# Optimization experiments

Hardware: AMD Instinct MI355X
Metric: run time of the kernel (lower is better)

## Reference

```python
import jax, jax.numpy as jnp
import numpy as np
import math

B, L, OBS, ACT = 2, 1024, 64, 16
OE, AE, RE, TE = 512, 256, 128, 128
C, H, NL, FF = 1024, 16, 4, 4096
DH = C // H


def setup_inputs():
    key = jax.random.key(0)
    ks = jax.random.split(key, 20)
    def nrm(k, shape, std=1.0):
        return jax.random.normal(k, shape, jnp.float32) * std
    kb = jax.random.split(ks[19], 12)
    return {
        'obs_seq': nrm(ks[0], (B, L, OBS)),
        'act_seq': nrm(ks[1], (B, L, ACT)),
        'rew_seq': nrm(ks[2], (B, L, 1)),
        'obs_W': nrm(ks[3], (OBS, OE), OBS ** -0.5), 'obs_b': jnp.zeros((OE,)),
        'act_W': nrm(ks[4], (ACT, AE), ACT ** -0.5), 'act_b': jnp.zeros((AE,)),
        'rew_W': nrm(ks[5], (1, RE), 1.0), 'rew_b': jnp.zeros((RE,)),
        'tr_W': nrm(ks[6], (OBS, TE), OBS ** -0.5), 'tr_b': jnp.zeros((TE,)),
        'bn_gamma': jnp.ones((OBS,)), 'bn_beta': jnp.zeros((OBS,)),
        'ln1_w': jnp.ones((NL, C)), 'ln1_b': jnp.zeros((NL, C)),
        'qkv_W': nrm(kb[0], (NL, C, 3 * C), C ** -0.5), 'qkv_b': jnp.zeros((NL, 3 * C)),
        'out_W': nrm(kb[1], (NL, C, C), C ** -0.5), 'out_b': jnp.zeros((NL, C)),
        'ln2_w': jnp.ones((NL, C)), 'ln2_b': jnp.zeros((NL, C)),
        'fc_W': nrm(kb[2], (NL, C, FF), C ** -0.5), 'fc_b': jnp.zeros((NL, FF)),
        'pj_W': nrm(kb[3], (NL, FF, C), FF ** -0.5), 'pj_b': jnp.zeros((NL, C)),
    }


def _ln(x, w, b):
    m = x.mean(-1, keepdims=True)
    v = ((x - m) ** 2).mean(-1, keepdims=True)
    return (x - m) * jax.lax.rsqrt(v + 1e-5) * w + b


def _forward(obs_seq, act_seq, rew_seq, obs_W, obs_b, act_W, act_b, rew_W, rew_b,
             tr_W, tr_b, bn_gamma, bn_beta, ln1_w, ln1_b, qkv_W, qkv_b, out_W, out_b,
             ln2_w, ln2_b, fc_W, fc_b, pj_W, pj_b):
    # transition branch: prepend first obs, take deltas; BatchNorm1d in training
    # mode uses biased batch stats over (batch, time) per channel.
    full_obs = jnp.concatenate([obs_seq[:, :1], obs_seq], axis=1)  # (B, L+1, OBS)
    obs2 = full_obs[:, :-1]
    tran = full_obs[:, 1:] - full_obs[:, :-1]  # (B, L, OBS)
    tm = tran.mean((0, 1))
    tv = ((tran - tm) ** 2).mean((0, 1))
    tran = (tran - tm) * jax.lax.rsqrt(tv + 1e-5) * bn_gamma + bn_beta
    # encoder_activation is identity
    enc = jnp.concatenate([
        obs2 @ obs_W + obs_b,
        act_seq @ act_W + act_b,
        rew_seq @ rew_W + rew_b,
        tran @ tr_W + tr_b,
    ], axis=-1)  # (B, L, C)
    mask = jnp.tril(jnp.ones((L, L), dtype=bool))

    def block(x, p):
        l1w, l1b, qW, qb, oW, ob, l2w, l2b, fW, fb, pW, pb = p
        h = _ln(x, l1w, l1b)
        q, k, v = jnp.split(h @ qW + qb, 3, axis=-1)
        q, k, v = (t.reshape(B, L, H, DH).transpose(0, 2, 1, 3) for t in (q, k, v))
        s = jnp.einsum('bhqd,bhkd->bhqk', q, k) / math.sqrt(DH)
        s = jnp.where(mask, s, -jnp.inf)
        a = jax.nn.softmax(s, axis=-1)
        o = jnp.einsum('bhqk,bhkd->bhqd', a, v).transpose(0, 2, 1, 3).reshape(B, L, C)
        x = x + o @ oW + ob  # residual + out_proj
        h2 = _ln(x, l2w, l2b)
        x = x + jax.nn.relu(h2 @ fW + fb) @ pW + pb  # MLP residual
        return x, None

    x, _ = jax.lax.scan(block, enc, (ln1_w, ln1_b, qkv_W, qkv_b, out_W, out_b,
                                     ln2_w, ln2_b, fc_W, fc_b, pj_W, pj_b))
    return jnp.tanh(x)


def reference(obs_seq, act_seq, rew_seq, obs_W, obs_b, act_W, act_b, rew_W, rew_b,
              tr_W, tr_b, bn_gamma, bn_beta, ln1_w, ln1_b, qkv_W, qkv_b, out_W, out_b,
              ln2_w, ln2_b, fc_W, fc_b, pj_W, pj_b):
    return _forward(obs_seq, act_seq, rew_seq, obs_W, obs_b, act_W, act_b, rew_W, rew_b,
                    tr_W, tr_b, bn_gamma, bn_beta, ln1_w, ln1_b, qkv_W, qkv_b, out_W, out_b,
                    ln2_w, ln2_b, fc_W, fc_b, pj_W, pj_b)
```

## Files before the change

### kernel.cpp

```cpp
#include <hip/hip_runtime.h>
#include <hip/hip_bf16.h>
#include <math.h>

constexpr int kB   = 2;
constexpr int kL   = 1024;
constexpr int kOBS = 64;
constexpr int kACT = 16;
constexpr int kC   = 1024;
constexpr int kH   = 16;
constexpr int kDH  = 64;
constexpr int kFF  = 4096;
constexpr int kNL  = 4;
constexpr int kRows = kB * kL;
constexpr int kOE = 512, kAE = 256, kRE = 128, kTE = 128;

typedef _Float16 f16x8 __attribute__((ext_vector_type(8)));
typedef _Float16 f16x4 __attribute__((ext_vector_type(4)));
typedef float    f32x4 __attribute__((ext_vector_type(4)));

__device__ __forceinline__ unsigned short f2h(float x) {
    return __builtin_bit_cast(unsigned short, (_Float16)x);
}
__device__ __forceinline__ void gload_lds16(const void* g, void* l) {
    __builtin_amdgcn_global_load_lds(
        (const __attribute__((address_space(1))) unsigned int*)g,
        (__attribute__((address_space(3))) unsigned int*)l, 16, 0, 0);
}

__global__ __launch_bounds__(256) void tran_stats_kernel(
    const float* __restrict__ obs, float* __restrict__ tm, float* __restrict__ tv)
{
    const int f = blockIdx.x;
    const int tid = threadIdx.x;
    float sum = 0.f, sq = 0.f;
    for (int r = tid; r < kRows; r += 256) {
        const int t = r & (kL - 1);
        float d = 0.f;
        if (t > 0) {
            const float cur  = obs[(size_t)r * kOBS + f];
            const float prev = obs[(size_t)(r - 1) * kOBS + f];
            d = cur - prev;
        }
        sum += d; sq += d * d;
    }
    for (int off = 32; off > 0; off >>= 1) {
        sum += __shfl_down(sum, off);
        sq  += __shfl_down(sq, off);
    }
    __shared__ float sa[4], sb[4];
    if ((tid & 63) == 0) { sa[tid >> 6] = sum; sb[tid >> 6] = sq; }
    __syncthreads();
    if (tid == 0) {
        const float ts = sa[0] + sa[1] + sa[2] + sa[3];
        const float tq = sb[0] + sb[1] + sb[2] + sb[3];
        const float m = ts / (float)kRows;
        tm[f] = m;
        tv[f] = tq / (float)kRows - m * m;
    }
}

__global__ __launch_bounds__(256) void encode_kernel(
    const float* __restrict__ obs, const float* __restrict__ act, const float* __restrict__ rew,
    const float* __restrict__ obs_W, const float* __restrict__ obs_b,
    const float* __restrict__ act_W, const float* __restrict__ act_b,
    const float* __restrict__ rew_W, const float* __restrict__ rew_b,
    const float* __restrict__ tr_W,  const float* __restrict__ tr_b,
    const float* __restrict__ bn_g,  const float* __restrict__ bn_b,
    const float* __restrict__ tm,    const float* __restrict__ tv,
    float* __restrict__ enc)
{
    const int row = blockIdx.x;
    const int t = row & (kL - 1);
    const int tid = threadIdx.x;
    __shared__ float s_obs2[kOBS];
    __shared__ float s_tran[kOBS];
    __shared__ float s_act[kACT];
    __shared__ float s_rew;
    if (tid < kOBS) {
        const float cur  = obs[(size_t)row * kOBS + tid];
        const float prev = (t > 0) ? obs[(size_t)(row - 1) * kOBS + tid] : cur;
        s_obs2[tid] = prev;
        const float tr = cur - prev;
        s_tran[tid] = (tr - tm[tid]) * rsqrtf(tv[tid] + 1e-5f) * bn_g[tid] + bn_b[tid];
    } else if (tid < kOBS + kACT) {
        s_act[tid - kOBS] = act[(size_t)row * kACT + (tid - kOBS)];
    } else if (tid == kOBS + kACT) {
        s_rew = rew[row];
    }
    __syncthreads();
    float* er = enc + (size_t)row * kC;
    #pragma unroll
    for (int s = 0; s < 4; ++s) {
        const int c = tid + s * 256;
        float v;
        if (c < kOE) {
            v = obs_b[c];
            #pragma unroll
            for (int k = 0; k < kOBS; ++k) v += s_obs2[k] * obs_W[k * kOE + c];
        } else if (c < kOE + kAE) {
            const int cc = c - kOE;
            v = act_b[cc];
            #pragma unroll
            for (int k = 0; k < kACT; ++k) v += s_act[k] * act_W[k * kAE + cc];
        } else if (c < kOE + kAE + kRE) {
            const int cc = c - (kOE + kAE);
            v = s_rew * rew_W[cc] + rew_b[cc];
        } else {
            const int cc = c - (kOE + kAE + kRE);
            v = tr_b[cc];
            #pragma unroll
            for (int k = 0; k < kOBS; ++k) v += s_tran[k] * tr_W[k * kTE + cc];
        }
        er[c] = v;
    }
}

__global__ __launch_bounds__(256) void ln_kernel(
    const float* __restrict__ x, const float* __restrict__ w,
    const float* __restrict__ b, unsigned short* __restrict__ out)
{
    const int row = blockIdx.x;
    const int tid = threadIdx.x;
    const float4 xv = *reinterpret_cast<const float4*>(&x[(size_t)row * kC + tid * 4]);
    float s = xv.x + xv.y + xv.z + xv.w;
    float q = xv.x * xv.x + xv.y * xv.y + xv.z * xv.z + xv.w * xv.w;
    for (int off = 32; off > 0; off >>= 1) {
        s += __shfl_down(s, off);
        q += __shfl_down(q, off);
    }
    __shared__ float sa[4], sb[4];
    if ((tid & 63) == 0) { sa[tid >> 6] = s; sb[tid >> 6] = q; }
    __syncthreads();
    const float ts = sa[0] + sa[1] + sa[2] + sa[3];
    const float tq = sb[0] + sb[1] + sb[2] + sb[3];
    const float mean = ts * (1.f / kC);
    const float var  = tq * (1.f / kC) - mean * mean;
    const float rstd = rsqrtf(var + 1e-5f);
    const float4 wv = *reinterpret_cast<const float4*>(&w[tid * 4]);
    const float4 bv = *reinterpret_cast<const float4*>(&b[tid * 4]);
    ushort4 o;
    o.x = f2h((xv.x - mean) * rstd * wv.x + bv.x);
    o.y = f2h((xv.y - mean) * rstd * wv.y + bv.y);
    o.z = f2h((xv.z - mean) * rstd * wv.z + bv.z);
    o.w = f2h((xv.w - mean) * rstd * wv.w + bv.w);
    *reinterpret_cast<ushort4*>(&out[(size_t)row * kC + tid * 4]) = o;
}

__device__ __forceinline__ void convT_tile(
    const float* __restrict__ W, unsigned short* __restrict__ WT,
    int K, int N, int k0, int n0, int tid)
{
    __shared__ unsigned short t[64][68];
    const int r = tid >> 4, c4 = (tid & 15) * 4;
    #pragma unroll
    for (int s = 0; s < 4; ++s) {
        const int rr = r + s * 16;
        const float4 v = *reinterpret_cast<const float4*>(&W[(size_t)(k0 + rr) * N + n0 + c4]);
        t[rr][c4 + 0] = f2h(v.x);
        t[rr][c4 + 1] = f2h(v.y);
        t[rr][c4 + 2] = f2h(v.z);
        t[rr][c4 + 3] = f2h(v.w);
    }
    __syncthreads();
    #pragma unroll
    for (int s = 0; s < 4; ++s) {
        const int rn = r + s * 16;
        ushort4 o;
        o.x = t[c4 + 0][rn];
        o.y = t[c4 + 1][rn];
        o.z = t[c4 + 2][rn];
        o.w = t[c4 + 3][rn];
        *reinterpret_cast<ushort4*>(&WT[(size_t)(n0 + rn) * K + k0 + c4]) = o;
    }
}

__global__ __launch_bounds__(256) void convert_layer_kernel(
    const float* __restrict__ qW, const float* __restrict__ oW,
    const float* __restrict__ fW, const float* __restrict__ pW,
    unsigned short* __restrict__ qWT, unsigned short* __restrict__ oWT,
    unsigned short* __restrict__ fWT, unsigned short* __restrict__ pWT)
{
    int bid = blockIdx.x;
    const int tid = threadIdx.x;
    if (bid < 768)  {
        convT_tile(qW, qWT, 1024, 3072, (bid / 48) * 64, (bid % 48) * 64, tid);
    } else if (bid < 1024) {
        bid -= 768;
        convT_tile(oW, oWT, 1024, 1024, (bid / 16) * 64, (bid % 16) * 64, tid);
    } else if (bid < 2048) {
        bid -= 1024;
        convT_tile(fW, fWT, 1024, 4096, (bid / 64) * 64, (bid % 64) * 64, tid);
    } else {
        bid -= 2048;
        convT_tile(pW, pWT, 4096, 1024, (bid / 16) * 64, (bid % 16) * 64, tid);
    }
}

template<int RELU, int RES, int MODE>
__global__ __launch_bounds__(256) void gemm_f16_kernel(
    const unsigned short* __restrict__ A,
    const unsigned short* __restrict__ BT,
    const float* __restrict__ bias,
    float* __restrict__ Cf, unsigned short* __restrict__ Ch,
    unsigned short* __restrict__ Cv,
    int M, int N, int K)
{
    __shared__ __align__(16) unsigned short As[2][128 * 64];
    __shared__ __align__(16) unsigned short Bs[2][128 * 64];
    const int tid = threadIdx.x;
    const int lane = tid & 63;
    const int wv   = tid >> 6;
    const int wr = wv >> 1, wc = wv & 1;

    const int nx  = gridDim.x;
    const int nxy = gridDim.x * gridDim.y;
    int flat = blockIdx.x + nx * blockIdx.y + nxy * blockIdx.z;
    const int cpx = (nxy * gridDim.z) >> 3;
    flat = (flat & 7) * cpx + (flat >> 3);
    const int bx = flat % nx;
    const int by = (flat / nx) % gridDim.y;
    const int bz = flat / nxy;

    const int bm = by * 128;
    const int bn = bx * 128;
    const int ksz  = K / gridDim.z;
    const int kbeg = bz * ksz;
    const int kend = kbeg + ksz;

    const int grow = tid >> 3;
    const int gs   = (tid & 7) ^ (grow & 7);

    const int fr = lane & 15;
    const int kb = lane >> 4;

    auto stage = [&](int k0, int buf) {
        #pragma unroll
        for (int c = 0; c < 4; ++c) {
            gload_lds16(A  + (size_t)(bm + c * 32 + grow) * K + k0 + gs * 8,
                        (char*)&As[buf][0] + c * 4096 + wv * 1024);
            gload_lds16(BT + (size_t)(bn + c * 32 + grow) * K + k0 + gs * 8,
                        (char*)&Bs[buf][0] + c * 4096 + wv * 1024);
        }
    };

    f32x4 acc[4][4] = {};

    stage(kbeg, 0);
    __syncthreads();
    int cur = 0;
    for (int k0 = kbeg; k0 < kend; k0 += 64) {
        if (k0 + 64 < kend) stage(k0 + 64, cur ^ 1);

        #pragma unroll
        for (int kf = 0; kf < 2; ++kf) {
            f16x8 a[4], b[4];
            #pragma unroll
            for (int m = 0; m < 4; ++m) {
                const int row = wr * 64 + m * 16 + fr;
                a[m] = *reinterpret_cast<const f16x8*>(
                    &As[cur][row * 64 + (((kf * 4 + kb) ^ (row & 7)) * 8)]);
            }
            #pragma unroll
            for (int n = 0; n < 4; ++n) {
                const int row = wc * 64 + n * 16 + fr;
                b[n] = *reinterpret_cast<const f16x8*>(
                    &Bs[cur][row * 64 + (((kf * 4 + kb) ^ (row & 7)) * 8)]);
            }
            #pragma unroll
            for (int m = 0; m < 4; ++m)
                #pragma unroll
                for (int n = 0; n < 4; ++n)
                    acc[m][n] = __builtin_amdgcn_mfma_f32_16x16x32_f16(a[m], b[n], acc[m][n], 0, 0, 0);
        }

        __syncthreads();
        cur ^= 1;
    }

    const int fq = lane >> 4;
    if (MODE == 4) {
        const bool addb = (bz == 0);
        #pragma unroll
        for (int n = 0; n < 4; ++n) {
            const int c = bn + wc * 64 + n * 16 + fr;
            const float bv = addb ? bias[c] : 0.f;
            #pragma unroll
            for (int m = 0; m < 4; ++m) {
                #pragma unroll
                for (int j = 0; j < 4; ++j) {
                    const int r = bm + wr * 64 + m * 16 + fq * 4 + j;
                    atomicAdd(&Cf[(size_t)r * N + c], acc[m][n][j] + bv);
                }
            }
        }
        return;
    }
    if (MODE == 2) {
        if (bn < 2 * kC) {
            #pragma unroll
            for (int n = 0; n < 4; ++n) {
                const int c = bn + wc * 64 + n * 16 + fr;
                const float bv = bias[c];
                #pragma unroll
                for (int m = 0; m < 4; ++m) {
                    #pragma unroll
                    for (int j = 0; j < 4; ++j) {
                        const int r = bm + wr * 64 + m * 16 + fq * 4 + j;
                        Ch[(size_t)r * (2 * kC) + c] = f2h(acc[m][n][j] + bv);
                    }
                }
            }
        } else {
            #pragma unroll
            for (int n = 0; n < 4; ++n) {
                const int c  = bn + wc * 64 + n * 16 + fr;
                const int cc = c - 2 * kC;
                const int hh = cc >> 6, dd = cc & 63;
                const float bv = bias[c];
                #pragma unroll
                for (int m = 0; m < 4; ++m) {
                    const int rr = bm + wr * 64 + m * 16 + fq * 4;
                    const int bb = rr >> 10, t0 = rr & 1023;
                    f16x4 pk;
                    #pragma unroll
                    for (int j = 0; j < 4; ++j) pk[j] = (_Float16)(acc[m][n][j] + bv);
                    *reinterpret_cast<f16x4*>(
                        &Cv[((size_t)(bb * kH + hh) * kDH + dd) * kL + t0]) = pk;
                }
            }
        }
        return;
    }
    #pragma unroll
    for (int n = 0; n < 4; ++n) {
        const int c = bn + wc * 64 + n * 16 + fr;
        const float bv = bias[c];
        #pragma unroll
        for (int m = 0; m < 4; ++m) {
            #pragma unroll
            for (int j = 0; j < 4; ++j) {
                const int r = bm + wr * 64 + m * 16 + fq * 4 + j;
                float v = acc[m][n][j] + bv;
                if (RES)  v += Cf[(size_t)r * N + c];
                if (RELU) v = fmaxf(v, 0.f);
                if (MODE == 1) Ch[(size_t)r * N + c] = f2h(v);
                else           Cf[(size_t)r * N + c] = v;
            }
        }
    }
}

__device__ __forceinline__ int swz(int row, int slot) {
    return row * 64 + ((slot ^ (row & 7)) * 8);
}

__global__ __launch_bounds__(256) void attn_mfma_kernel(
    const unsigned short* __restrict__ qk,
    const unsigned short* __restrict__ vt,
    unsigned short* __restrict__ o)
{
    const int bid = blockIdx.x;
    const int bh  = bid & 31;
    const int qb  = ((bid >> 5) + bh) & 15;
    const int b   = bh >> 4;
    const int h   = bh & 15;
    const int tid  = threadIdx.x;
    const int lane = tid & 63;
    const int wv   = tid >> 6;
    const int fr = lane & 15;
    const int g  = lane >> 4;

    __shared__ __align__(16) unsigned short Qs[64 * 64];
    __shared__ __align__(16) unsigned short Ks[64 * 64];
    __shared__ __align__(16) unsigned short Vts[64 * 64];
    __shared__ __align__(16) unsigned short Ps[64 * 64];

    const int qlo = qb * 64;

    {
        const int r = tid >> 2, s = tid & 3;
        const unsigned short* qg = &qk[(size_t)(b * kL + qlo + r) * (2 * kC) + h * kDH];
        f16x8 v0 = *reinterpret_cast<const f16x8*>(&qg[s * 8]);
        f16x8 v1 = *reinterpret_cast<const f16x8*>(&qg[(s + 4) * 8]);
        #pragma unroll
        for (int i = 0; i < 8; ++i) { v0[i] *= (_Float16)0.125f; v1[i] *= (_Float16)0.125f; }
        *reinterpret_cast<f16x8*>(&Qs[swz(r, s)])     = v0;
        *reinterpret_cast<f16x8*>(&Qs[swz(r, s + 4)]) = v1;
    }
    __syncthreads();

    f16x8 qfrag[2];
    #pragma unroll
    for (int kf = 0; kf < 2; ++kf)
        qfrag[kf] = *reinterpret_cast<const f16x8*>(&Qs[swz(wv * 16 + fr, kf * 4 + g)]);

    float m = -INFINITY, l = 0.f;
    f32x4 acc_o[4] = {};
    const int qg_row = qlo + wv * 16 + fr;

    for (int k0 = 0; k0 <= qlo; k0 += 64) {
        __syncthreads();
        {
            const int r = tid >> 2, s = tid & 3;
            const unsigned short* kg = &qk[(size_t)(b * kL + k0 + r) * (2 * kC) + kC + h * kDH];
            *reinterpret_cast<f16x8*>(&Ks[swz(r, s)])     = *reinterpret_cast<const f16x8*>(&kg[s * 8]);
            *reinterpret_cast<f16x8*>(&Ks[swz(r, s + 4)]) = *reinterpret_cast<const f16x8*>(&kg[(s + 4) * 8]);
            const unsigned short* vg = &vt[((size_t)(b * kH + h) * kDH + r) * kL + k0];
            *reinterpret_cast<f16x8*>(&Vts[swz(r, s)])     = *reinterpret_cast<const f16x8*>(&vg[s * 8]);
            *reinterpret_cast<f16x8*>(&Vts[swz(r, s + 4)]) = *reinterpret_cast<const f16x8*>(&vg[(s + 4) * 8]);
        }
        __syncthreads();

        f32x4 acc_s[4] = {};
        #pragma unroll
        for (int kf = 0; kf < 2; ++kf) {
            const f16x8 qf = qfrag[kf];
            #pragma unroll
            for (int n = 0; n < 4; ++n) {
                const f16x8 kfr = *reinterpret_cast<const f16x8*>(&Ks[swz(n * 16 + fr, kf * 4 + g)]);
                acc_s[n] = __builtin_amdgcn_mfma_f32_16x16x32_f16(kfr, qf, acc_s[n], 0, 0, 0);
            }
        }

        if (k0 == qlo) {
            #pragma unroll
            for (int n = 0; n < 4; ++n)
                #pragma unroll
                for (int j = 0; j < 4; ++j)
                    if (k0 + n * 16 + g * 4 + j > qg_row) acc_s[n][j] = -INFINITY;
        }

        float mx = -INFINITY;
        #pragma unroll
        for (int n = 0; n < 4; ++n)
            #pragma unroll
            for (int j = 0; j < 4; ++j) mx = fmaxf(mx, acc_s[n][j]);
        mx = fmaxf(mx, __shfl_xor(mx, 16));
        mx = fmaxf(mx, __shfl_xor(mx, 32));
        const float mn  = fmaxf(m, mx);
        const float fac = __expf(m - mn);
        float p[4][4];
        float psum = 0.f;
        #pragma unroll
        for (int n = 0; n < 4; ++n)
            #pragma unroll
            for (int j = 0; j < 4; ++j) { p[n][j] = __expf(acc_s[n][j] - mn); psum += p[n][j]; }
        psum += __shfl_xor(psum, 16);
        psum += __shfl_xor(psum, 32);
        l = l * fac + psum;
        m = mn;
        #pragma unroll
        for (int dt = 0; dt < 4; ++dt)
            #pragma unroll
            for (int j = 0; j < 4; ++j) acc_o[dt][j] *= fac;

        #pragma unroll
        for (int n = 0; n < 4; ++n) {
            f16x4 pk;
            #pragma unroll
            for (int j = 0; j < 4; ++j) pk[j] = (_Float16)p[n][j];
            *reinterpret_cast<f16x4*>(&Ps[swz(wv * 16 + fr, 2 * n + (g >> 1)) + (g & 1) * 4]) = pk;
        }

        #pragma unroll
        for (int kf = 0; kf < 2; ++kf) {
            const f16x8 pf = *reinterpret_cast<const f16x8*>(&Ps[swz(wv * 16 + fr, kf * 4 + g)]);
            #pragma unroll
            for (int dt = 0; dt < 4; ++dt) {
                const f16x8 vf = *reinterpret_cast<const f16x8*>(&Vts[swz(dt * 16 + fr, kf * 4 + g)]);
                acc_o[dt] = __builtin_amdgcn_mfma_f32_16x16x32_f16(vf, pf, acc_o[dt], 0, 0, 0);
            }
        }
    }

    const float rl = 1.f / l;
    unsigned short* ob = &o[(size_t)(b * kL + qg_row) * kC + h * kDH];
    #pragma unroll
    for (int dt = 0; dt < 4; ++dt) {
        f16x4 pk;
        #pragma unroll
        for (int j = 0; j < 4; ++j) pk[j] = (_Float16)(acc_o[dt][j] * rl);
        *reinterpret_cast<f16x4*>(&ob[dt * 16 + g * 4]) = pk;
    }
}

__global__ __launch_bounds__(256) void tanh_kernel(float* __restrict__ x)
{
    const size_t i = ((size_t)blockIdx.x * 256 + threadIdx.x) * 4;
    float4 v = *reinterpret_cast<float4*>(&x[i]);
    v.x = tanhf(v.x); v.y = tanhf(v.y); v.z = tanhf(v.z); v.w = tanhf(v.w);
    *reinterpret_cast<float4*>(&x[i]) = v;
}

extern "C" void kernel_launch(void* const* d_in, const int* in_sizes, int n_in,
                              void* d_out, int out_size, void* d_ws, size_t ws_size,
                              hipStream_t stream)
{
    (void)in_sizes; (void)n_in; (void)out_size; (void)ws_size;
    const float* obs    = (const float*)d_in[0];
    const float* act    = (const float*)d_in[1];
    const float* rew    = (const float*)d_in[2];
    const float* obs_W  = (const float*)d_in[3];
    const float* obs_b  = (const float*)d_in[4];
    const float* act_W  = (const float*)d_in[5];
    const float* act_b  = (const float*)d_in[6];
    const float* rew_W  = (const float*)d_in[7];
    const float* rew_b  = (const float*)d_in[8];
    const float* tr_W   = (const float*)d_in[9];
    const float* tr_b   = (const float*)d_in[10];
    const float* bn_g   = (const float*)d_in[11];
    const float* bn_b   = (const float*)d_in[12];
    const float* ln1_w  = (const float*)d_in[13];
    const float* ln1_b  = (const float*)d_in[14];
    const float* qkv_W  = (const float*)d_in[15];
    const float* qkv_b  = (const float*)d_in[16];
    const float* out_W  = (const float*)d_in[17];
    const float* out_b  = (const float*)d_in[18];
    const float* ln2_w  = (const float*)d_in[19];
    const float* ln2_b  = (const float*)d_in[20];
    const float* fc_W   = (const float*)d_in[21];
    const float* fc_b   = (const float*)d_in[22];
    const float* pj_W   = (const float*)d_in[23];
    const float* pj_b   = (const float*)d_in[24];

    float* x  = (float*)d_out;
    float* ws = (float*)d_ws;
    float* tm   = ws;
    float* tv   = ws + 64;
    unsigned short* wbuf  = (unsigned short*)(ws + 128);
    unsigned short* h_hf  = wbuf + 12582912;
    unsigned short* ao_hf = h_hf + (size_t)kRows * kC;
    unsigned short* ff_hf = ao_hf + (size_t)kRows * kC;
    unsigned short* qk_hf = ff_hf + (size_t)kRows * kFF;
    unsigned short* vt_hf = qk_hf + (size_t)kRows * 2 * kC;
    unsigned short* qWT = wbuf;
    unsigned short* oWT = qWT + 3 * kC * kC;
    unsigned short* fWT = oWT + kC * kC;
    unsigned short* pWT = fWT + kC * kFF;

    tran_stats_kernel<<<kOBS, 256, 0, stream>>>(obs, tm, tv);
    encode_kernel<<<kRows, 256, 0, stream>>>(obs, act, rew,
        obs_W, obs_b, act_W, act_b, rew_W, rew_b, tr_W, tr_b, bn_g, bn_b, tm, tv, x);

    for (int lyr = 0; lyr < kNL; ++lyr) {
        const float* qW = qkv_W + (size_t)lyr * kC * 3 * kC;
        const float* qB = qkv_b + (size_t)lyr * 3 * kC;
        const float* oW = out_W + (size_t)lyr * kC * kC;
        const float* oB = out_b + (size_t)lyr * kC;
        const float* fW = fc_W + (size_t)lyr * kC * kFF;
        const float* fB = fc_b + (size_t)lyr * kFF;
        const float* pW = pj_W + (size_t)lyr * kFF * kC;
        const float* pB = pj_b + (size_t)lyr * kC;

        convert_layer_kernel<<<3072, 256, 0, stream>>>(
            qW, oW, fW, pW, qWT, oWT, fWT, pWT);

        ln_kernel<<<kRows, 256, 0, stream>>>(x, ln1_w + lyr * kC, ln1_b + lyr * kC, h_hf);
        gemm_f16_kernel<0,0,2><<<dim3(3 * kC / 128, kRows / 128), 256, 0, stream>>>(
            h_hf, qWT, qB, nullptr, qk_hf, vt_hf, kRows, 3 * kC, kC);
        attn_mfma_kernel<<<dim3(512), 256, 0, stream>>>(qk_hf, vt_hf, ao_hf);
        gemm_f16_kernel<0,0,4><<<dim3(kC / 128, kRows / 128, 4), 256, 0, stream>>>(
            ao_hf, oWT, oB, x, nullptr, nullptr, kRows, kC, kC);
        ln_kernel<<<kRows, 256, 0, stream>>>(x, ln2_w + lyr * kC, ln2_b + lyr * kC, h_hf);
        gemm_f16_kernel<1,0,1><<<dim3(kFF / 128, kRows / 128), 256, 0, stream>>>(
            h_hf, fWT, fB, nullptr, ff_hf, nullptr, kRows, kFF, kC);
        gemm_f16_kernel<0,0,4><<<dim3(kC / 128, kRows / 128, 4), 256, 0, stream>>>(
            ff_hf, pWT, pB, x, nullptr, nullptr, kRows, kC, kFF);
    }
    tanh_kernel<<<kRows * kC / 1024, 256, 0, stream>>>(x);
}
```

Measured before the change: 685.8 us.

## Switch GEMM to triple-buffered BK=32 pipeline with explicit vmcnt waits

Restructures the f16 MFMA GEMM main loop from a double-buffered BK=64 scheme to a triple-buffered BK=32 scheme. Global-to-LDS loads run two stages ahead, and each iteration waits with explicit s_waitcnt vmcnt counts and a single s_barrier. The LDS swizzle is adjusted to the 32-wide rows. The aim is to hide global load latency and cut LDS footprint so occupancy can rise, at the cost of more barriers per unit of K and hand-tuned waitcnt counts that depend on the exact number of outstanding loads.

```diff
diff --git a/kernel.cpp b/kernel.cpp
--- a/kernel.cpp
+++ b/kernel.cpp
@@ -205,8 +205,8 @@
     unsigned short* __restrict__ Cv,
     int M, int N, int K)
 {
-    __shared__ __align__(16) unsigned short As[2][128 * 64];
-    __shared__ __align__(16) unsigned short Bs[2][128 * 64];
+    __shared__ __align__(16) unsigned short As[3][128 * 32];
+    __shared__ __align__(16) unsigned short Bs[3][128 * 32];
     const int tid = threadIdx.x;
     const int lane = tid & 63;
     const int wv   = tid >> 6;
@@ -227,54 +227,64 @@
     const int kbeg = bz * ksz;
     const int kend = kbeg + ksz;
 
-    const int grow = tid >> 3;
-    const int gs   = (tid & 7) ^ (grow & 7);
+    const int grow = tid >> 2;
+    const int gs   = (tid & 3) ^ ((tid >> 3) & 3);
 
     const int fr = lane & 15;
     const int kb = lane >> 4;
 
     auto stage = [&](int k0, int buf) {
-        #pragma unroll
-        for (int c = 0; c < 4; ++c) {
-            gload_lds16(A  + (size_t)(bm + c * 32 + grow) * K + k0 + gs * 8,
-                        (char*)&As[buf][0] + c * 4096 + wv * 1024);
-            gload_lds16(BT + (size_t)(bn + c * 32 + grow) * K + k0 + gs * 8,
-                        (char*)&Bs[buf][0] + c * 4096 + wv * 1024);
-        }
+        gload_lds16(A  + (size_t)(bm + grow) * K + k0 + gs * 8,
+                    (char*)&As[buf][0] + wv * 1024);
+        gload_lds16(A  + (size_t)(bm + 64 + grow) * K + k0 + gs * 8,
+                    (char*)&As[buf][0] + 4096 + wv * 1024);
+        gload_lds16(BT + (size_t)(bn + grow) * K + k0 + gs * 8,
+                    (char*)&Bs[buf][0] + wv * 1024);
+        gload_lds16(BT + (size_t)(bn + 64 + grow) * K + k0 + gs * 8,
+                    (char*)&Bs[buf][0] + 4096 + wv * 1024);
     };
 
     f32x4 acc[4][4] = {};
 
     stage(kbeg, 0);
-    __syncthreads();
+    if (kbeg + 32 < kend) stage(kbeg + 32, 1);
     int cur = 0;
-    for (int k0 = kbeg; k0 < kend; k0 += 64) {
-        if (k0 + 64 < kend) stage(k0 + 64, cur ^ 1);
-
-        #pragma unroll
-        for (int kf = 0; kf < 2; ++kf) {
-            f16x8 a[4], b[4];
-            #pragma unroll
-            for (int m = 0; m < 4; ++m) {
-                const int row = wr * 64 + m * 16 + fr;
-                a[m] = *reinterpret_cast<const f16x8*>(
-                    &As[cur][row * 64 + (((kf * 4 + kb) ^ (row & 7)) * 8)]);
-            }
-            #pragma unroll
-            for (int n = 0; n < 4; ++n) {
-                const int row = wc * 64 + n * 16 + fr;
-                b[n] = *reinterpret_cast<const f16x8*>(
-                    &Bs[cur][row * 64 + (((kf * 4 + kb) ^ (row & 7)) * 8)]);
-            }
-            #pragma unroll
-            for (int m = 0; m < 4; ++m)
-                #pragma unroll
-                for (int n = 0; n < 4; ++n)
-                    acc[m][n] = __builtin_amdgcn_mfma_f32_16x16x32_f16(a[m], b[n], acc[m][n], 0, 0, 0);
-        }
-
-        __syncthreads();
-        cur ^= 1;
+    for (int k0 = kbeg; k0 < kend; k0 += 32) {
+        if (k0 + 32 < kend) {
+            asm volatile("s_waitcnt vmcnt(4)" ::: "memory");
+        } else {
+            asm volatile("s_waitcnt vmcnt(0)" ::: "memory");
+        }
+        asm volatile("s_waitcnt lgkmcnt(0)" ::: "memory");
+        __builtin_amdgcn_sched_barrier(0);
+        __builtin_amdgcn_s_barrier();
+        __builtin_amdgcn_sched_barrier(0);
+
+        f16x8 a[4], b[4];
+        #pragma unroll
+        for (int m = 0; m < 4; ++m) {
+            const int row = wr * 64 + m * 16 + fr;
+            a[m] = *reinterpret_cast<const f16x8*>(
+                &As[cur][row * 32 + ((kb ^ ((row >> 1) & 3)) * 8)]);
+        }
+        #pragma unroll
+        for (int n = 0; n < 4; ++n) {
+            const int row = wc * 64 + n * 16 + fr;
+            b[n] = *reinterpret_cast<const f16x8*>(
+                &Bs[cur][row * 32 + ((kb ^ ((row >> 1) & 3)) * 8)]);
+        }
+        if (k0 + 64 < kend) {
+            int sb = cur + 2; if (sb >= 3) sb -= 3;
+            stage(k0 + 64, sb);
+        }
+        #pragma unroll
+        for (int m = 0; m < 4; ++m)
+            #pragma unroll
+            for (int n = 0; n < 4; ++n)
+                acc[m][n] = __builtin_amdgcn_mfma_f32_16x16x32_f16(
+                    a[m], b[n], acc[m][n], 0, 0, 0);
+
+        ++cur; if (cur >= 3) cur = 0;
     }
 
     const int fq = lane >> 4;
```

New measurement: 690.2 us. About the same (+0.6%).
